# Optimization experiments

Measured on AMD Instinct MI355X. Metric: run time of the kernel, lower is better.

The kernel has to match this reference:

```python
import jax, jax.numpy as jnp
import numpy as np

EPS = 1e-8

def l2norm(x, axis=-1):
    norm = jnp.sqrt(jnp.sum(x * x, axis=axis, keepdims=True)) + EPS
    return x / norm


def setup_inputs() -> dict:
    key = jax.random.key(0)
    ks = jax.random.split(key, 16)
    B, N, IMG_DIM, EMBED = 256, 36, 2048, 1024
    DK = EMBED // 8  # 128
    H3 = 3 * EMBED
    r_wl = float(np.sqrt(6.0) / np.sqrt(IMG_DIM + EMBED))
    r_k = float(np.sqrt(6.0) / np.sqrt(EMBED + DK))
    r_v = float(np.sqrt(6.0) / np.sqrt(EMBED + EMBED))
    sg = 1.0 / np.sqrt(EMBED)  # torch GRU default init range
    return {
        "images": jax.random.normal(ks[0], (B, N, IMG_DIM), jnp.float32),
        "oimages": jax.random.normal(ks[1], (B, EMBED), jnp.float32),
        "wl_w": jax.random.uniform(ks[2], (EMBED, IMG_DIM), jnp.float32, -r_wl, r_wl),
        "wl_b": jnp.zeros((EMBED,), jnp.float32),
        "wk_w": jax.random.uniform(ks[3], (DK, EMBED), jnp.float32, -r_k, r_k),
        "wk_b": jnp.zeros((DK,), jnp.float32),
        "wq_w": jax.random.uniform(ks[4], (DK, EMBED), jnp.float32, -r_k, r_k),
        "wq_b": jnp.zeros((DK,), jnp.float32),
        "wv_w": jax.random.uniform(ks[5], (EMBED, EMBED), jnp.float32, -r_v, r_v),
        "wv_b": jnp.zeros((EMBED,), jnp.float32),
        "gru_wih": jax.random.uniform(ks[6], (H3, EMBED), jnp.float32, -sg, sg),
        "gru_whh": jax.random.uniform(ks[7], (H3, EMBED), jnp.float32, -sg, sg),
        "gru_bih": jax.random.uniform(ks[8], (H3,), jnp.float32, -sg, sg),
        "gru_bhh": jax.random.uniform(ks[9], (H3,), jnp.float32, -sg, sg),
    }


def gru_last_hidden(x, wih, whh, bih, bhh):
    # Single-layer batch_first GRU (torch gate order r, z, n); returns final hidden h_N.
    B, N, H = x.shape[0], x.shape[1], whh.shape[1]
    gi = jnp.einsum('bnd,gd->bng', x, wih) + bih  # (B, N, 3H), input gates precomputed

    def step(h, gi_t):
        gh = h @ whh.T + bhh
        ir, iz, inn = jnp.split(gi_t, 3, axis=-1)
        hr, hz, hn = jnp.split(gh, 3, axis=-1)
        r = jax.nn.sigmoid(ir + hr)
        z = jax.nn.sigmoid(iz + hz)
        n = jnp.tanh(inn + r * hn)
        h_new = (1.0 - z) * n + z * h
        return h_new, None

    h0 = jnp.zeros((B, H), x.dtype)
    hN, _ = jax.lax.scan(step, h0, jnp.swapaxes(gi, 0, 1))
    return hN


def reference(images, oimages, wl_w, wl_b, wk_w, wk_b, wq_w, wq_b, wv_w, wv_b,
              gru_wih, gru_whh, gru_bih, gru_bhh):
    dk = wk_w.shape[0]
    f = jnp.einsum('bni,ei->bne', images, wl_w) + wl_b      # (B, N, E)
    f = l2norm(f, axis=-1)
    f = f + oimages[:, None, :]                              # broadcast add

    k = jnp.einsum('bne,de->bnd', f, wk_w) + wk_b            # (B, N, dk)
    q = jnp.einsum('bne,de->bnd', f, wq_w) + wq_b            # (B, N, dk)
    scores = jnp.einsum('bid,bjd->bij', k, q) / jnp.sqrt(jnp.asarray(dk, f.dtype))
    w_mn = jax.nn.softmax(scores, axis=2)                    # (B, N, N)
    v = jnp.einsum('bne,de->bnd', f, wv_w) + wv_b            # (B, N, E)
    # Original torch code: (w_mn[b,i,j] * v[b,i,d]).sum(j) -> v scaled by row-sums
    # of the softmax (== 1). Expressed faithfully without the BxNxNxE intermediate:
    attn = jnp.sum(w_mn, axis=2)[..., None] * v              # == v
    f = attn + f

    hN = gru_last_hidden(f, gru_wih, gru_whh, gru_bih, gru_bhh)  # out[:, N-1, :]
    return l2norm(hN, axis=-1)
```

## Files before the change

### kernel.cpp

```cpp
#include <hip/hip_runtime.h>
#include <hip/hip_bf16.h>

#define DEVI __device__ __forceinline__

typedef short bf16x8 __attribute__((ext_vector_type(8)));
typedef float f32x4 __attribute__((ext_vector_type(4)));

#define NBLK_G 128


DEVI unsigned short f2b(float f) {
    union { float f; unsigned u; } x; x.f = f;
    unsigned r = x.u + 0x7fffu + ((x.u >> 16) & 1u);
    return (unsigned short)(r >> 16);
}

DEVI float b2f(unsigned short u) {
    union { unsigned u; float f; } x; x.u = ((unsigned)u) << 16; return x.f;
}

DEVI void gld_lds16(const void* g, void* l) {
    __builtin_amdgcn_global_load_lds(
        (const __attribute__((address_space(1))) void*)g,
        (__attribute__((address_space(3))) void*)l, 16, 0, 0);
}

DEVI bf16x8 cp_load16(const void* p) {
    bf16x8 r;
    asm volatile("global_load_dwordx4 %0, %1, off sc0 sc1 nt"
                 : "=v"(r) : "v"(p) : "memory");
    return r;
}
DEVI void cp_store2(void* p, unsigned short v) {
    unsigned vv = v;
    asm volatile("global_store_short %0, %1, off sc0 sc1 nt"
                 :: "v"(p), "v"(vv) : "memory");
}


__global__ __launch_bounds__(256) void cvt_f32_bf16(
    const float* __restrict__ src, unsigned short* __restrict__ dst, int n4)
{
    int stride = gridDim.x * 256;
    for (int i = blockIdx.x * 256 + threadIdx.x; i < n4; i += stride) {
        float4 v = reinterpret_cast<const float4*>(src)[i];
        ushort4 o;
        o.x = f2b(v.x); o.y = f2b(v.y); o.z = f2b(v.z); o.w = f2b(v.w);
        reinterpret_cast<ushort4*>(dst)[i] = o;
    }
}


template<int EPI>
__global__ __launch_bounds__(256) void gemm_bt(
    const unsigned short* __restrict__ A, const unsigned short* __restrict__ Bm,
    const float* __restrict__ bias, const float* resid,
    float* outF, unsigned short* outB,
    int Mn, int Nn, int K, int mtiles)
{
    __shared__ short lds[2][2][128 * 32];
    const int tid = threadIdx.x;
    const int lane = tid & 63, w = tid >> 6;
    const int bid = blockIdx.x;
    const int mt = bid % mtiles, nt = bid / mtiles;
    const int m0 = mt * 128, n0 = nt * 128;
    const int fr = lane & 15, kg = lane >> 4;
    const int wr = (w >> 1) * 64, wc = (w & 1) * 64;

    auto stage = [&](int buf, int k0) {
#pragma unroll
        for (int rnd = 0; rnd < 2; ++rnd) {
            int chunk = rnd * 256 + w * 64;
            int slot = chunk + lane;
            int row = slot >> 2, ks = slot & 3;
            gld_lds16(A + (size_t)(m0 + row) * K + k0 + ks * 8,
                      (void*)&lds[buf][0][chunk * 8]);
        }
#pragma unroll
        for (int rnd = 0; rnd < 2; ++rnd) {
            int chunk = rnd * 256 + w * 64;
            int slot = chunk + lane;
            int row = slot >> 2, ks = slot & 3;
            gld_lds16(Bm + (size_t)(n0 + row) * K + k0 + ks * 8,
                      (void*)&lds[buf][1][chunk * 8]);
        }
    };

    f32x4 acc[4][4] = {};

    stage(0, 0);
    __syncthreads();
    const int nk = K >> 5;
    for (int kt = 0; kt < nk; ++kt) {
        int buf = kt & 1;
        if (kt + 1 < nk) stage(buf ^ 1, (kt + 1) * 32);
        const short* As = lds[buf][0];
        const short* Bs = lds[buf][1];
        bf16x8 af[4], bfv[4];
#pragma unroll
        for (int m = 0; m < 4; ++m)
            af[m] = *(const bf16x8*)&As[(wr + m * 16 + fr) * 32 + kg * 8];
#pragma unroll
        for (int n = 0; n < 4; ++n)
            bfv[n] = *(const bf16x8*)&Bs[(wc + n * 16 + fr) * 32 + kg * 8];
#pragma unroll
        for (int m = 0; m < 4; ++m)
#pragma unroll
            for (int n = 0; n < 4; ++n)
                acc[m][n] = __builtin_amdgcn_mfma_f32_16x16x32_bf16(
                    af[m], bfv[n], acc[m][n], 0, 0, 0);
        __syncthreads();
    }

#pragma unroll
    for (int n = 0; n < 4; ++n) {
        int col = n0 + wc + n * 16 + fr;
        float bc = bias[col];
#pragma unroll
        for (int m = 0; m < 4; ++m) {
            f32x4 v = acc[m][n];
#pragma unroll
            for (int i = 0; i < 4; ++i) {
                int row = m0 + wr + m * 16 + kg * 4 + i;
                float val = v[i] + bc;
                if (EPI == 0) {
                    outF[(size_t)row * Nn + col] = val;
                } else if (EPI == 2) {
                    size_t idx = (size_t)row * Nn + col;
                    val += resid[idx];
                    outB[idx] = f2b(val);
                } else {
                    int b = row / 36, t = row - b * 36;
                    outB[(size_t)(t * 256 + b) * Nn + col] = f2b(val);
                }
            }
        }
    }
}


__global__ __launch_bounds__(256) void l2norm_add(
    const float* fin, const float* __restrict__ oimg,
    float* foutF, unsigned short* __restrict__ foutB)
{
    int row = blockIdx.x;
    int b = row / 36;
    float4 v = reinterpret_cast<const float4*>(fin + (size_t)row * 1024)[threadIdx.x];
    float s = v.x * v.x + v.y * v.y + v.z * v.z + v.w * v.w;
#pragma unroll
    for (int o = 32; o; o >>= 1) s += __shfl_down(s, o, 64);
    __shared__ float ws4[4];
    int lane = threadIdx.x & 63, w = threadIdx.x >> 6;
    if (lane == 0) ws4[w] = s;
    __syncthreads();
    float tot = ws4[0] + ws4[1] + ws4[2] + ws4[3];
    float inv = 1.0f / (sqrtf(tot) + 1e-8f);
    float4 o4 = reinterpret_cast<const float4*>(oimg + (size_t)b * 1024)[threadIdx.x];
    float4 y;
    y.x = v.x * inv + o4.x; y.y = v.y * inv + o4.y;
    y.z = v.z * inv + o4.z; y.w = v.w * inv + o4.w;
    reinterpret_cast<float4*>(foutF + (size_t)row * 1024)[threadIdx.x] = y;
    ushort4 yb; yb.x = f2b(y.x); yb.y = f2b(y.y); yb.z = f2b(y.z); yb.w = f2b(y.w);
    reinterpret_cast<ushort4*>(foutB + (size_t)row * 1024)[threadIdx.x] = yb;
}


__global__ __launch_bounds__(512, 2) void gru_persist(
    const unsigned short* __restrict__ whhB,
    const unsigned short* __restrict__ giB,
    const float* __restrict__ bhh,
    unsigned short* hA,
    unsigned short* hBb,
    float* __restrict__ hfin,
    unsigned* bar)
{
    __shared__ short whs[48 * 1024];
    const int tid = threadIdx.x, lane = tid & 63, w = tid >> 6;
    const int bid = blockIdx.x;
    const int c = bid >> 1, p = bid & 1;
    const int e0 = c * 16;
    const int fr = lane & 15, kg = lane >> 4;
    const int szk = fr & 7;

    for (int it = 0; it < 12; ++it) {
        int slot = it * 512 + tid;
        int j = slot >> 7, pc = slot & 127;
        int gc = pc ^ (j & 7);
        int grow = (j >> 4) * 1024 + e0 + (j & 15);
        gld_lds16(whhB + (size_t)grow * 1024 + gc * 8, (void*)&whs[slot * 8]);
    }
    __syncthreads();

    const int e = e0 + fr;
    const float bhr = bhh[e], bhz = bhh[1024 + e], bhn = bhh[2048 + e];
    float hreg[4] = {0.f, 0.f, 0.f, 0.f};
    int bb[4];
#pragma unroll
    for (int i = 0; i < 4; ++i) bb[i] = p * 128 + w * 16 + kg * 4 + i;
    const int arow = p * 128 + w * 16 + fr;
    unsigned* cnt = &bar[p * 32];

    unsigned short* hbuf[2] = { hA, hBb };

    for (int t = 0; t < 36; ++t) {
        const unsigned short* hc = hbuf[t & 1];
        unsigned short* hn = hbuf[(t + 1) & 1];

        const unsigned short* hrow = hc + (size_t)arow * 1024 + kg * 8;
        bf16x8 av[32];
#pragma unroll
        for (int kt = 0; kt < 32; ++kt)
            av[kt] = cp_load16(hrow + kt * 32);

        const unsigned short* gbase = giB + (size_t)t * 256 * 3072 + e;
        unsigned short giu[4][3];
#pragma unroll
        for (int i = 0; i < 4; ++i) {
            const unsigned short* g = gbase + (size_t)bb[i] * 3072;
            giu[i][0] = g[0]; giu[i][1] = g[1024]; giu[i][2] = g[2048];
        }

        asm volatile("s_waitcnt vmcnt(0)" ::: "memory");
        __builtin_amdgcn_sched_barrier(0);

        f32x4 a0 = {}, a1 = {}, a2 = {};
#pragma unroll
        for (int kt = 0; kt < 32; ++kt) {
            const int pc0 = ((kt * 4 + kg) ^ szk) << 3;
            bf16x8 w0 = *(const bf16x8*)&whs[(0 * 16 + fr) * 1024 + pc0];
            a0 = __builtin_amdgcn_mfma_f32_16x16x32_bf16(av[kt], w0, a0, 0, 0, 0);
            bf16x8 w1 = *(const bf16x8*)&whs[(1 * 16 + fr) * 1024 + pc0];
            a1 = __builtin_amdgcn_mfma_f32_16x16x32_bf16(av[kt], w1, a1, 0, 0, 0);
            bf16x8 w2 = *(const bf16x8*)&whs[(2 * 16 + fr) * 1024 + pc0];
            a2 = __builtin_amdgcn_mfma_f32_16x16x32_bf16(av[kt], w2, a2, 0, 0, 0);
        }

#pragma unroll
        for (int i = 0; i < 4; ++i) {
            float ir = b2f(giu[i][0]), iz = b2f(giu[i][1]), inn = b2f(giu[i][2]);
            float r = 1.f / (1.f + __expf(-(ir + a0[i] + bhr)));
            float z = 1.f / (1.f + __expf(-(iz + a1[i] + bhz)));
            float n = tanhf(inn + r * (a2[i] + bhn));
            hreg[i] = (1.f - z) * n + z * hreg[i];
        }

        if (t == 35) {
#pragma unroll
            for (int i = 0; i < 4; ++i)
                hfin[(size_t)bb[i] * 1024 + e] = hreg[i];
        } else {
#pragma unroll
            for (int i = 0; i < 4; ++i)
                cp_store2(&hn[(size_t)bb[i] * 1024 + e], f2b(hreg[i]));
            asm volatile("s_waitcnt vmcnt(0)" ::: "memory");
            __syncthreads();
            if (tid == 0) {
                __hip_atomic_fetch_add(cnt, 1u, __ATOMIC_RELAXED,
                                       __HIP_MEMORY_SCOPE_AGENT);
                const unsigned target = 64u * (unsigned)(t + 1);
                int guard = 0;
                while (__hip_atomic_load(cnt, __ATOMIC_RELAXED,
                                         __HIP_MEMORY_SCOPE_AGENT) < target) {
                    __builtin_amdgcn_s_sleep(1);
                    if (++guard > (1 << 24)) break;
                }
            }
            __syncthreads();
        }
    }
}

__global__ __launch_bounds__(256) void zero_state(
    unsigned short* hb0, unsigned* bar)
{
    int i = blockIdx.x * 256 + threadIdx.x;
    if (i < 256 * 1024) hb0[i] = 0;
    if (i < 8192) bar[i] = 0;
}

__global__ __launch_bounds__(256) void final_norm(
    const float* __restrict__ hf, float* __restrict__ out)
{
    int row = blockIdx.x;
    float4 v = reinterpret_cast<const float4*>(hf + (size_t)row * 1024)[threadIdx.x];
    float s = v.x * v.x + v.y * v.y + v.z * v.z + v.w * v.w;
#pragma unroll
    for (int o = 32; o; o >>= 1) s += __shfl_down(s, o, 64);
    __shared__ float ws4[4];
    int lane = threadIdx.x & 63, w = threadIdx.x >> 6;
    if (lane == 0) ws4[w] = s;
    __syncthreads();
    float tot = ws4[0] + ws4[1] + ws4[2] + ws4[3];
    float inv = 1.0f / (sqrtf(tot) + 1e-8f);
    float4 y; y.x = v.x * inv; y.y = v.y * inv; y.z = v.z * inv; y.w = v.w * inv;
    reinterpret_cast<float4*>(out + (size_t)row * 1024)[threadIdx.x] = y;
}


extern "C" void kernel_launch(void* const* d_in, const int* in_sizes, int n_in,
                              void* d_out, int out_size, void* d_ws, size_t ws_size,
                              hipStream_t stream)
{
    constexpr int cB = 256, cN = 36, cIMG = 2048, cE = 1024, cH3 = 3072;
    constexpr int cM = cB * cN;

    const float* images  = (const float*)d_in[0];
    const float* oimages = (const float*)d_in[1];
    const float* wl_w    = (const float*)d_in[2];
    const float* wl_b    = (const float*)d_in[3];
    const float* wv_w    = (const float*)d_in[8];
    const float* wv_b    = (const float*)d_in[9];
    const float* wih     = (const float*)d_in[10];
    const float* whh     = (const float*)d_in[11];
    const float* bih     = (const float*)d_in[12];
    const float* bhh     = (const float*)d_in[13];

    char* ws = (char*)d_ws;
    size_t off = 0;
    auto alloc = [&](size_t bytes) -> char* {
        char* p = ws + off; off += (bytes + 255) & ~(size_t)255; return p;
    };
    unsigned short* imgB = (unsigned short*)alloc((size_t)cM * cIMG * 2);
    unsigned short* wlB  = (unsigned short*)alloc((size_t)cE * cIMG * 2);
    unsigned short* wvB  = (unsigned short*)alloc((size_t)cE * cE * 2);
    unsigned short* wihB = (unsigned short*)alloc((size_t)cH3 * cE * 2);
    unsigned short* whhB = (unsigned short*)alloc((size_t)cH3 * cE * 2);
    float*          fpre = (float*)alloc((size_t)cM * cE * 4);
    unsigned short* fB   = (unsigned short*)alloc((size_t)cM * cE * 2);
    unsigned short* f2B  = (unsigned short*)alloc((size_t)cM * cE * 2);
    unsigned short* giB  = (unsigned short*)alloc((size_t)cM * cH3 * 2);
    float*          hfin = (float*)alloc((size_t)cB * cE * 4);
    unsigned short* hb0  = (unsigned short*)alloc((size_t)cB * cE * 2);
    unsigned short* hb1  = (unsigned short*)alloc((size_t)cB * cE * 2);
    unsigned*       bar  = (unsigned*)alloc(8192 * 4);
    (void)ws_size;

    cvt_f32_bf16<<<2048, 256, 0, stream>>>(images, imgB, cM * cIMG / 4);
    cvt_f32_bf16<<<512, 256, 0, stream>>>(wl_w, wlB, cE * cIMG / 4);
    cvt_f32_bf16<<<256, 256, 0, stream>>>(wv_w, wvB, cE * cE / 4);
    cvt_f32_bf16<<<512, 256, 0, stream>>>(wih, wihB, cH3 * cE / 4);
    cvt_f32_bf16<<<512, 256, 0, stream>>>(whh, whhB, cH3 * cE / 4);

    gemm_bt<0><<<72 * 8, 256, 0, stream>>>(imgB, wlB, wl_b, nullptr,
                                           fpre, nullptr, cM, cE, cIMG, 72);
    l2norm_add<<<cM, 256, 0, stream>>>(fpre, oimages, fpre, fB);

    gemm_bt<2><<<72 * 8, 256, 0, stream>>>(fB, wvB, wv_b, fpre,
                                           nullptr, f2B, cM, cE, cE, 72);
    gemm_bt<3><<<72 * 24, 256, 0, stream>>>(f2B, wihB, bih, nullptr,
                                            nullptr, giB, cM, cH3, cE, 72);

    zero_state<<<1024, 256, 0, stream>>>(hb0, bar);

    void* args[] = { (void*)&whhB, (void*)&giB, (void*)&bhh, (void*)&hb0,
                     (void*)&hb1, (void*)&hfin, (void*)&bar };
    hipLaunchCooperativeKernel((void*)gru_persist, dim3(NBLK_G), dim3(512),
                               args, 0, stream);

    final_norm<<<cB, 256, 0, stream>>>(hfin, (float*)d_out);
}
```

Baseline: 849.0 us.

## Split GRU batch over 256 single-CU blocks, use per-step hidden buffers and gate layout

The persistent GRU kernel now runs 256 blocks of 256 threads, each covering 64 batch rows, instead of 128 blocks of 512. The previous design held two blocks per CU sharing LDS, and the new split spreads the recurrent weight slices across more CUs. The hidden state is written to a fresh buffer for each timestep, reusing the image workspace. Because a step never reads a buffer that another block is still overwriting, h can be read with ordinary cached loads instead of cache-bypassing ones. The input-gate tensor is stored transposed so each thread fetches its four batch values with one vector load per gate. The risks are that whh is replicated four times across CUs, increasing L2 traffic, and that barrier groups are smaller but more numerous.

```diff
diff --git a/kernel.cpp b/kernel.cpp
--- a/kernel.cpp
+++ b/kernel.cpp
@@ -5,8 +5,6 @@
 
 typedef short bf16x8 __attribute__((ext_vector_type(8)));
 typedef float f32x4 __attribute__((ext_vector_type(4)));
-
-#define NBLK_G 128
 
 
 DEVI unsigned short f2b(float f) {
@@ -25,12 +23,6 @@
         (__attribute__((address_space(3))) void*)l, 16, 0, 0);
 }
 
-DEVI bf16x8 cp_load16(const void* p) {
-    bf16x8 r;
-    asm volatile("global_load_dwordx4 %0, %1, off sc0 sc1 nt"
-                 : "=v"(r) : "v"(p) : "memory");
-    return r;
-}
 DEVI void cp_store2(void* p, unsigned short v) {
     unsigned vv = v;
     asm volatile("global_store_short %0, %1, off sc0 sc1 nt"
@@ -131,7 +123,9 @@
                     outB[idx] = f2b(val);
                 } else {
                     int b = row / 36, t = row - b * 36;
-                    outB[(size_t)(t * 256 + b) * Nn + col] = f2b(val);
+                    int g = col >> 10, cc = (col >> 4) & 63, ce = col & 15;
+                    outB[((((size_t)t * 3 + g) * 64 + cc) * 16 + ce) * 256 + b]
+                        = f2b(val);
                 }
             }
         }
@@ -165,25 +159,24 @@
 }
 
 
-__global__ __launch_bounds__(512, 2) void gru_persist(
+__global__ __launch_bounds__(256, 1) void gru_persist(
     const unsigned short* __restrict__ whhB,
     const unsigned short* __restrict__ giB,
     const float* __restrict__ bhh,
-    unsigned short* hA,
-    unsigned short* hBb,
+    unsigned short* __restrict__ hseq,
     float* __restrict__ hfin,
     unsigned* bar)
 {
     __shared__ short whs[48 * 1024];
     const int tid = threadIdx.x, lane = tid & 63, w = tid >> 6;
     const int bid = blockIdx.x;
-    const int c = bid >> 1, p = bid & 1;
+    const int c = bid >> 2, rg = bid & 3;
     const int e0 = c * 16;
     const int fr = lane & 15, kg = lane >> 4;
     const int szk = fr & 7;
 
-    for (int it = 0; it < 12; ++it) {
-        int slot = it * 512 + tid;
+    for (int it = 0; it < 24; ++it) {
+        int slot = it * 256 + tid;
         int j = slot >> 7, pc = slot & 127;
         int gc = pc ^ (j & 7);
         int grow = (j >> 4) * 1024 + e0 + (j & 15);
@@ -194,34 +187,25 @@
     const int e = e0 + fr;
     const float bhr = bhh[e], bhz = bhh[1024 + e], bhn = bhh[2048 + e];
     float hreg[4] = {0.f, 0.f, 0.f, 0.f};
-    int bb[4];
-#pragma unroll
-    for (int i = 0; i < 4; ++i) bb[i] = p * 128 + w * 16 + kg * 4 + i;
-    const int arow = p * 128 + w * 16 + fr;
-    unsigned* cnt = &bar[p * 32];
-
-    unsigned short* hbuf[2] = { hA, hBb };
+    const int bb0 = rg * 64 + w * 16 + kg * 4;
+    const int arow = rg * 64 + w * 16 + fr;
+    unsigned* cnt = &bar[rg * 32];
 
     for (int t = 0; t < 36; ++t) {
-        const unsigned short* hc = hbuf[t & 1];
-        unsigned short* hn = hbuf[(t + 1) & 1];
+        const unsigned short* hc = hseq + (size_t)t * 262144;
+        unsigned short* hn = hseq + (size_t)(t + 1) * 262144;
 
         const unsigned short* hrow = hc + (size_t)arow * 1024 + kg * 8;
         bf16x8 av[32];
 #pragma unroll
         for (int kt = 0; kt < 32; ++kt)
-            av[kt] = cp_load16(hrow + kt * 32);
-
-        const unsigned short* gbase = giB + (size_t)t * 256 * 3072 + e;
-        unsigned short giu[4][3];
-#pragma unroll
-        for (int i = 0; i < 4; ++i) {
-            const unsigned short* g = gbase + (size_t)bb[i] * 3072;
-            giu[i][0] = g[0]; giu[i][1] = g[1024]; giu[i][2] = g[2048];
-        }
-
-        asm volatile("s_waitcnt vmcnt(0)" ::: "memory");
-        __builtin_amdgcn_sched_barrier(0);
+            av[kt] = *(const bf16x8*)(hrow + kt * 32);
+
+        union { ushort4 v; unsigned short u[4]; } gv[3];
+#pragma unroll
+        for (int g = 0; g < 3; ++g)
+            gv[g].v = *(const ushort4*)(
+                giB + ((((size_t)t * 3 + g) * 64 + c) * 16 + fr) * 256 + bb0);
 
         f32x4 a0 = {}, a1 = {}, a2 = {};
 #pragma unroll
@@ -237,7 +221,7 @@
 
 #pragma unroll
         for (int i = 0; i < 4; ++i) {
-            float ir = b2f(giu[i][0]), iz = b2f(giu[i][1]), inn = b2f(giu[i][2]);
+            float ir = b2f(gv[0].u[i]), iz = b2f(gv[1].u[i]), inn = b2f(gv[2].u[i]);
             float r = 1.f / (1.f + __expf(-(ir + a0[i] + bhr)));
             float z = 1.f / (1.f + __expf(-(iz + a1[i] + bhz)));
             float n = tanhf(inn + r * (a2[i] + bhn));
@@ -247,11 +231,11 @@
         if (t == 35) {
 #pragma unroll
             for (int i = 0; i < 4; ++i)
-                hfin[(size_t)bb[i] * 1024 + e] = hreg[i];
+                hfin[(size_t)(bb0 + i) * 1024 + e] = hreg[i];
         } else {
 #pragma unroll
             for (int i = 0; i < 4; ++i)
-                cp_store2(&hn[(size_t)bb[i] * 1024 + e], f2b(hreg[i]));
+                cp_store2(&hn[(size_t)(bb0 + i) * 1024 + e], f2b(hreg[i]));
             asm volatile("s_waitcnt vmcnt(0)" ::: "memory");
             __syncthreads();
             if (tid == 0) {
@@ -271,10 +255,10 @@
 }
 
 __global__ __launch_bounds__(256) void zero_state(
-    unsigned short* hb0, unsigned* bar)
+    unsigned short* h0, unsigned* bar)
 {
     int i = blockIdx.x * 256 + threadIdx.x;
-    if (i < 256 * 1024) hb0[i] = 0;
+    if (i < 256 * 1024) h0[i] = 0;
     if (i < 8192) bar[i] = 0;
 }
 
@@ -330,9 +314,8 @@
     unsigned short* f2B  = (unsigned short*)alloc((size_t)cM * cE * 2);
     unsigned short* giB  = (unsigned short*)alloc((size_t)cM * cH3 * 2);
     float*          hfin = (float*)alloc((size_t)cB * cE * 4);
-    unsigned short* hb0  = (unsigned short*)alloc((size_t)cB * cE * 2);
-    unsigned short* hb1  = (unsigned short*)alloc((size_t)cB * cE * 2);
     unsigned*       bar  = (unsigned*)alloc(8192 * 4);
+    unsigned short* hseq = imgB;
     (void)ws_size;
 
     cvt_f32_bf16<<<2048, 256, 0, stream>>>(images, imgB, cM * cIMG / 4);
@@ -350,11 +333,11 @@
     gemm_bt<3><<<72 * 24, 256, 0, stream>>>(f2B, wihB, bih, nullptr,
                                             nullptr, giB, cM, cH3, cE, 72);
 
-    zero_state<<<1024, 256, 0, stream>>>(hb0, bar);
-
-    void* args[] = { (void*)&whhB, (void*)&giB, (void*)&bhh, (void*)&hb0,
-                     (void*)&hb1, (void*)&hfin, (void*)&bar };
-    hipLaunchCooperativeKernel((void*)gru_persist, dim3(NBLK_G), dim3(512),
+    zero_state<<<1024, 256, 0, stream>>>(hseq, bar);
+
+    void* args[] = { (void*)&whhB, (void*)&giB, (void*)&bhh, (void*)&hseq,
+                     (void*)&hfin, (void*)&bar };
+    hipLaunchCooperativeKernel((void*)gru_persist, dim3(256), dim3(256),
                                args, 0, stream);
 
     final_norm<<<cB, 256, 0, stream>>>(hfin, (float*)d_out);
```

Result: faster. 816.0 us (-3.9%).
